# Optimization experiments

Hardware: AMD Instinct MI355X
Metric: run time of the kernel (lower is better)

## Reference

```python
import jax, jax.numpy as jnp
import numpy as np

B, C, H, W, E = 2, 4, 56, 56, 768
NH = 12
HD = E // NH
WS = 14
MLP_DIM = 3072
EPS = 1e-5


def layernorm(x, w, b):
    mu = jnp.mean(x, axis=-1, keepdims=True)
    var = jnp.mean((x - mu) ** 2, axis=-1, keepdims=True)
    return (x - mu) * jax.lax.rsqrt(var + EPS) * w + b


def setup_inputs() -> dict:
    key = jax.random.key(0)
    ks = jax.random.split(key, 12)
    s = 0.02
    return {
        "x": jax.random.normal(ks[0], (B, C, H, W, E), dtype=jnp.float32),
        "norm1_w": jnp.ones((E,), jnp.float32),
        "norm1_b": jnp.zeros((E,), jnp.float32),
        "qkv_w": jax.random.normal(ks[1], (E, 3 * E), jnp.float32) * s,
        "qkv_b": jnp.zeros((3 * E,), jnp.float32),
        "proj_w": jax.random.normal(ks[2], (E, E), jnp.float32) * s,
        "proj_b": jnp.zeros((E,), jnp.float32),
        "rel_pos_h": jax.random.normal(ks[3], (2 * WS - 1, HD), jnp.float32) * s,
        "rel_pos_w": jax.random.normal(ks[4], (2 * WS - 1, HD), jnp.float32) * s,
        "norm2_w": jnp.ones((E,), jnp.float32),
        "norm2_b": jnp.zeros((E,), jnp.float32),
        "mlp_w1": jax.random.normal(ks[5], (E, MLP_DIM), jnp.float32) * s,
        "mlp_b1": jnp.zeros((MLP_DIM,), jnp.float32),
        "mlp_w2": jax.random.normal(ks[6], (MLP_DIM, E), jnp.float32) * s,
        "mlp_b2": jnp.zeros((E,), jnp.float32),
    }


def reference(x, norm1_w, norm1_b, qkv_w, qkv_b, proj_w, proj_b,
              rel_pos_h, rel_pos_w, norm2_w, norm2_b,
              mlp_w1, mlp_b1, mlp_w2, mlp_b2):
    b, c, h, w, e = x.shape
    scale = HD ** -0.5
    shortcut = x

    y = x.reshape(b * c, h, w, e)
    y = layernorm(y, norm1_w, norm1_b)

    pad_h = (-h) % WS
    pad_w = (-w) % WS
    if pad_h or pad_w:
        y = jnp.pad(y, ((0, 0), (0, pad_h), (0, pad_w), (0, 0)))
    hp, wp = h + pad_h, w + pad_w
    y = y.reshape(b * c, hp // WS, WS, wp // WS, WS, e)
    y = y.transpose(0, 1, 3, 2, 4, 5).reshape(-1, WS, WS, e)  # [Bw, WS, WS, E]
    bw = y.shape[0]
    n = WS * WS

    # qkv projection
    qkv = y.reshape(bw, n, e) @ qkv_w + qkv_b
    qkv = qkv.reshape(bw, n, 3, NH, HD).transpose(2, 0, 3, 1, 4).reshape(3, bw * NH, n, HD)
    q, k, v = qkv[0], qkv[1], qkv[2]

    attn = (q * scale) @ jnp.swapaxes(k, -2, -1)  # [bw*NH, n, n]

    # decomposed relative position bias (q_size == k_size == WS, no interpolation)
    idx = jnp.arange(WS)[:, None] - jnp.arange(WS)[None, :] + (WS - 1)  # [WS, WS]
    Rh = rel_pos_h[idx]  # [WS, WS, HD]
    Rw = rel_pos_w[idx]
    r_q = q.reshape(-1, WS, WS, HD)
    rel_h = jnp.einsum('bhwc,hkc->bhwk', r_q, Rh)
    rel_w = jnp.einsum('bhwc,wkc->bhwk', r_q, Rw)
    attn = (attn.reshape(-1, WS, WS, WS, WS)
            + rel_h[..., :, None]
            + rel_w[:, :, :, None, :]).reshape(-1, n, n)

    attn = jax.nn.softmax(attn, axis=-1)
    out = attn @ v  # [bw*NH, n, HD]
    out = out.reshape(bw, NH, WS, WS, HD).transpose(0, 2, 3, 1, 4).reshape(bw, WS, WS, e)
    out = out @ proj_w + proj_b

    # window unpartition
    out = out.reshape(b * c, hp // WS, wp // WS, WS, WS, e)
    out = out.transpose(0, 1, 3, 2, 4, 5).reshape(b * c, hp, wp, e)
    out = out[:, :h, :w, :].reshape(b, c, h, w, e)

    x1 = shortcut + out
    z = layernorm(x1, norm2_w, norm2_b)
    z = jax.nn.gelu(z @ mlp_w1 + mlp_b1, approximate=False)
    z = z @ mlp_w2 + mlp_b2
    return x1 + z
```

## Files before the change

### kernel.cpp

```cpp
#include <hip/hip_runtime.h>
#include <math.h>

typedef unsigned short u16;
typedef __bf16 bf16x8 __attribute__((ext_vector_type(8)));
typedef float   f32x4 __attribute__((ext_vector_type(4)));
typedef u16     u16x4 __attribute__((ext_vector_type(4)));

#define TOK 25088
#define EMB 768
#define NWH 1536
#define NTOKW 196
#define PROW 224
#define PPAD 232
#define GROUP_M 4

#define OFF_VT 38535168ull
#define OFF_W0 127565824ull
#define OFF_W1 131104768ull
#define OFF_W2 132284416ull
#define OFF_W3 137003008ull
#define OFF_H  38535168ull

__device__ __forceinline__ u16 f2bf(float f) {
  __bf16 h = (__bf16)f;
  return __builtin_bit_cast(u16, h);
}

__device__ __forceinline__ float bf2f(u16 u) {
  return __builtin_bit_cast(float, (unsigned)u << 16);
}

__device__ __forceinline__ void cp16(void* lds, const void* gsrc) {
  __builtin_amdgcn_global_load_lds((const __attribute__((address_space(1))) void*)gsrc,
                                   (__attribute__((address_space(3))) void*)lds,
                                   16, 0, 0);
}

__device__ __forceinline__ f32x4 mfma16(bf16x8 a, bf16x8 b, f32x4 c) {
  return __builtin_amdgcn_mfma_f32_16x16x32_bf16(a, b, c, 0, 0, 0);
}

__device__ __forceinline__ void map_block(int b, int nwg, int nbm, int nbn,
                                          int* bm, int* bn) {
  const int q = nwg >> 3, r = nwg & 7;
  const int xcd = b & 7, slot = b >> 3;
  const int logical = (xcd < r ? xcd * (q + 1) : r * (q + 1) + (xcd - r) * q) + slot;
  const int in_group = GROUP_M * nbn;
  const int gid = logical / in_group;
  const int rem0 = logical - gid * in_group;
  const int gm = min(GROUP_M, nbm - gid * GROUP_M);
  *bm = gid * GROUP_M + rem0 % gm;
  *bn = rem0 / gm;
}

__global__ __launch_bounds__(256)
void transpose_w(const float* __restrict__ src, u16* __restrict__ dst, int R, int C) {
  __shared__ float tile[32][33];
  const int tx = threadIdx.x & 31;
  const int ty = threadIdx.x >> 5;
  const int c0 = blockIdx.x * 32;
  const int r0 = blockIdx.y * 32;
  #pragma unroll
  for (int i = ty; i < 32; i += 8)
    tile[i][tx] = src[(size_t)(r0 + i) * C + c0 + tx];
  __syncthreads();
  #pragma unroll
  for (int i = ty; i < 32; i += 8)
    dst[(size_t)(c0 + i) * R + r0 + tx] = f2bf(tile[tx][i]);
}

template<bool WIN>
__global__ __launch_bounds__(256)
void ln_kernel(const float* __restrict__ x, const float* __restrict__ g,
               const float* __restrict__ b, u16* __restrict__ y) {
  const int wave = threadIdx.x >> 6;
  const int lane = threadIdx.x & 63;
  const int row = blockIdx.x * 4 + wave;
  const float* xr = x + (size_t)row * EMB;
  float4 v[3];
  float s = 0.f, ss = 0.f;
  #pragma unroll
  for (int j = 0; j < 3; j++) {
    v[j] = *(const float4*)&xr[lane * 4 + j * 256];
    s  += v[j].x + v[j].y + v[j].z + v[j].w;
    ss += v[j].x*v[j].x + v[j].y*v[j].y + v[j].z*v[j].z + v[j].w*v[j].w;
  }
  #pragma unroll
  for (int off = 1; off < 64; off <<= 1) {
    s  += __shfl_xor(s, off);
    ss += __shfl_xor(ss, off);
  }
  const float mu = s * (1.0f / 768.0f);
  const float var = ss * (1.0f / 768.0f) - mu * mu;
  const float rs = rsqrtf(var + 1e-5f);
  size_t drow;
  if (WIN) {
    const int bc = row / 3136;
    const int rem = row - bc * 3136;
    const int h = rem / 56;
    const int w = rem - h * 56;
    const int window = bc * 16 + (h / 14) * 4 + (w / 14);
    const int token = (h % 14) * 14 + (w % 14);
    drow = (size_t)window * NTOKW + token;
  } else {
    drow = (size_t)row;
  }
  u16* yr = y + drow * EMB;
  #pragma unroll
  for (int j = 0; j < 3; j++) {
    const int e = lane * 4 + j * 256;
    const float4 gv = *(const float4*)&g[e];
    const float4 bv = *(const float4*)&b[e];
    u16x4 o;
    o[0] = f2bf((v[j].x - mu) * rs * gv.x + bv.x);
    o[1] = f2bf((v[j].y - mu) * rs * gv.y + bv.y);
    o[2] = f2bf((v[j].z - mu) * rs * gv.z + bv.z);
    o[3] = f2bf((v[j].w - mu) * rs * gv.w + bv.w);
    *(u16x4*)&yr[e] = o;
  }
}

#define EPI_QKV  0
#define EPI_PROJ 1
#define EPI_MLP1 2
#define EPI_MLP2 3

template<int EPI>
__global__ __launch_bounds__(512, 2)
void gemm256(const u16* __restrict__ A, const u16* __restrict__ Bt,
             int K, int moff, int nbm, int nbn,
             const float* __restrict__ bias,
             const float* __restrict__ aux,
             u16* __restrict__ o0, u16* __restrict__ o1, u16* __restrict__ o2,
             float* of) {
  __shared__ __align__(16) u16 lds[2][2][256 * 64];
  const int t = threadIdx.x;
  const int wave = t >> 6;
  const int lane = t & 63;
  const int quad = lane >> 4;
  const int l16 = lane & 15;
  const int wm = wave >> 2;
  const int wn = wave & 3;

  int bm, bn;
  map_block(blockIdx.x, gridDim.x, nbm, nbn, &bm, &bn);
  const int m0 = bm * 256;
  const int n0 = bn * 256;

  const int sr0 = t >> 3;
  const int sc0 = ((t ^ (t >> 3)) & 7) * 8;
  const int c1_ = t + 512;
  const int sr1 = c1_ >> 3;
  const int sc1 = ((c1_ ^ (c1_ >> 3)) & 7) * 8;
  const u16* Ag0 = A + (size_t)(m0 + sr0) * K + sc0;
  const u16* Ag1 = A + (size_t)(m0 + sr1) * K + sc1;
  const u16* Bg0 = Bt + (size_t)(n0 + sr0) * K + sc0;
  const u16* Bg1 = Bt + (size_t)(n0 + sr1) * K + sc1;
  const size_t hstep = (size_t)128 * K;

  const int cK0 = ((quad    ) ^ (l16 & 7)) * 8;
  const int cK1 = ((4 + quad) ^ (l16 & 7)) * 8;

  f32x4 acc[8][4];
  const f32x4 zero4 = {0.f, 0.f, 0.f, 0.f};
  #pragma unroll
  for (int i = 0; i < 8; i++)
    #pragma unroll
    for (int j = 0; j < 4; j++) acc[i][j] = zero4;
  bf16x8 bfr[4][2];

#define STG(bb, mat, half, G0, G1, kk) do {                                          \
    cp16(&lds[bb][mat][(half) * 8192 + wave * 512],        (G0) + (half) * hstep + (kk)); \
    cp16(&lds[bb][mat][(half) * 8192 + 4096 + wave * 512], (G1) + (half) * hstep + (kk)); \
  } while (0)

#define LOADB(bb) do {                                                               \
    _Pragma("unroll")                                                                \
    for (int nf = 0; nf < 4; nf++) {                                                 \
      bfr[nf][0] = *(const bf16x8*)&lds[bb][1][(wn * 64 + nf * 16 + l16) * 64 + cK0];\
      bfr[nf][1] = *(const bf16x8*)&lds[bb][1][(wn * 64 + nf * 16 + l16) * 64 + cK1];\
    }                                                                                \
  } while (0)

#define PHASE(bb, slab, PRE, POST) do {                                              \
    const int ar_ = (wm * 128 + (slab) * 32 + l16) * 64;                             \
    bf16x8 a00 = *(const bf16x8*)&lds[bb][0][ar_ + cK0];                             \
    bf16x8 a01 = *(const bf16x8*)&lds[bb][0][ar_ + cK1];                             \
    bf16x8 a10 = *(const bf16x8*)&lds[bb][0][ar_ + 1024 + cK0];                      \
    bf16x8 a11 = *(const bf16x8*)&lds[bb][0][ar_ + 1024 + cK1];                      \
    PRE;                                                                             \
    __builtin_amdgcn_s_barrier();                                                    \
    asm volatile("s_waitcnt lgkmcnt(0)" ::: "memory");                               \
    __builtin_amdgcn_sched_barrier(0);                                               \
    __builtin_amdgcn_s_setprio(1);                                                   \
    _Pragma("unroll")                                                                \
    for (int nf = 0; nf < 4; nf++) {                                                 \
      acc[(slab) * 2    ][nf] = mfma16(a00, bfr[nf][0], acc[(slab) * 2    ][nf]);    \
      acc[(slab) * 2    ][nf] = mfma16(a01, bfr[nf][1], acc[(slab) * 2    ][nf]);    \
      acc[(slab) * 2 + 1][nf] = mfma16(a10, bfr[nf][0], acc[(slab) * 2 + 1][nf]);    \
      acc[(slab) * 2 + 1][nf] = mfma16(a11, bfr[nf][1], acc[(slab) * 2 + 1][nf]);    \
    }                                                                                \
    __builtin_amdgcn_s_setprio(0);                                                   \
    POST;                                                                            \
    __builtin_amdgcn_s_barrier();                                                    \
  } while (0)

  STG(0, 1, 0, Bg0, Bg1, 0);  STG(0, 1, 1, Bg0, Bg1, 0);
  STG(0, 0, 0, Ag0, Ag1, 0);  STG(0, 0, 1, Ag0, Ag1, 0);
  STG(1, 1, 0, Bg0, Bg1, 64); STG(1, 1, 1, Bg0, Bg1, 64);
  asm volatile("s_waitcnt vmcnt(4)" ::: "memory");
  __builtin_amdgcn_s_barrier();

  const int T = K >> 7;
  for (int it = 0; it < T; ++it) {
    const bool nlast = (it < T - 1);
    const int kA1 = (2 * it + 1) << 6;
    const int kT2 = (2 * it + 2) << 6;
    const int kT3 = (2 * it + 3) << 6;

    LOADB(0);
    PHASE(0, 0, STG(1, 0, 0, Ag0, Ag1, kA1), );
    PHASE(0, 1, STG(1, 0, 1, Ag0, Ag1, kA1), );
    PHASE(0, 2, if (nlast) STG(0, 1, 0, Bg0, Bg1, kT2), );
    PHASE(0, 3, if (nlast) STG(0, 1, 1, Bg0, Bg1, kT2),
          if (nlast) { asm volatile("s_waitcnt vmcnt(4)" ::: "memory"); }
          else       { asm volatile("s_waitcnt vmcnt(0)" ::: "memory"); }
          __builtin_amdgcn_sched_barrier(0); );
    LOADB(1);
    PHASE(1, 0, if (nlast) STG(0, 0, 0, Ag0, Ag1, kT2), );
    PHASE(1, 1, if (nlast) STG(0, 0, 1, Ag0, Ag1, kT2), );
    PHASE(1, 2, if (nlast) STG(1, 1, 0, Bg0, Bg1, kT3), );
    PHASE(1, 3, if (nlast) STG(1, 1, 1, Bg0, Bg1, kT3),
          asm volatile("s_waitcnt vmcnt(4)" ::: "memory");
          __builtin_amdgcn_sched_barrier(0); );
  }
#undef STG
#undef LOADB
#undef PHASE

  #pragma unroll
  for (int mf = 0; mf < 8; mf++) {
    const int mb = m0 + wm * 128 + mf * 16 + quad * 4;
    #pragma unroll
    for (int nf = 0; nf < 4; nf++) {
      const int n = n0 + wn * 64 + nf * 16 + l16;
      const float bn_ = bias[n];
      if (EPI == EPI_QKV) {
        const int j3 = n / 768;
        const int rem = n - j3 * 768;
        const int head = rem >> 6;
        const int d = rem & 63;
        if (j3 == 2) {
          const int window = mb / 196;
          const int token = mb - window * 196;
          const int wh = window * 12 + head;
          u16x4 pv;
          #pragma unroll
          for (int r = 0; r < 4; r++) pv[r] = f2bf(acc[mf][nf][r] + bn_);
          *(u16x4*)&o2[((size_t)wh * 64 + d) * PROW + token] = pv;
        } else {
          u16* dst = (j3 == 0) ? o0 : o1;
          #pragma unroll
          for (int r = 0; r < 4; r++) {
            const int m = mb + r;
            const int window = m / 196;
            const int token = m - window * 196;
            const int wh = window * 12 + head;
            dst[((size_t)wh * NTOKW + token) * 64 + d] = f2bf(acc[mf][nf][r] + bn_);
          }
        }
      } else if (EPI == EPI_MLP1) {
        #pragma unroll
        for (int r = 0; r < 4; r++) {
          const int m = mb + r;
          float v = acc[mf][nf][r] + bn_;
          v = 0.5f * v * (1.0f + erff(v * 0.70710678118654752f));
          o0[(size_t)m * 3072 + n] = f2bf(v);
        }
      }
    }
  }
}

template<int EPI>
__global__ __launch_bounds__(256, 3)
void gemm_bt(const u16* __restrict__ A, const u16* __restrict__ Bt,
             int K, int moff, int nbm, int nbn,
             const float* __restrict__ bias,
             const float* __restrict__ aux,
             u16* __restrict__ o0,
             float* of) {
  __shared__ __align__(16) u16 lsA[4096];
  __shared__ __align__(16) u16 lsB[4096];
  const int t = threadIdx.x;
  const int wave = t >> 6;
  const int lane = t & 63;
  const int quad = lane >> 4;
  const int l16 = lane & 15;

  int bm, bn;
  map_block(blockIdx.x, gridDim.x, nbm, nbn, &bm, &bn);
  const int m0 = bm * 128;
  const int n0 = bn * 128;

  const int wm = (wave >> 1) * 64;
  const int wn = (wave & 1) * 64;

  const int srow = t >> 2;
  const int scol = (((t & 3) ^ ((t >> 3) & 3))) * 8;
  const u16* Ag = A + (size_t)(m0 + srow) * K + scol;
  const u16* Bg = Bt + (size_t)(n0 + srow) * K + scol;
  u16* lA0 = lsA + wave * 512;
  u16* lA1 = lsA + 2048 + wave * 512;
  u16* lB0 = lsB + wave * 512;
  u16* lB1 = lsB + 2048 + wave * 512;

  const int kc = (quad ^ ((l16 >> 1) & 3)) * 8;

  f32x4 acc[4][4];
  const f32x4 zero4 = {0.f, 0.f, 0.f, 0.f};
  #pragma unroll
  for (int i = 0; i < 4; i++)
    #pragma unroll
    for (int j = 0; j < 4; j++) acc[i][j] = zero4;

  for (int k0 = 0; k0 < K; k0 += 32) {
    cp16(lA0, Ag + k0);
    cp16(lA1, Ag + (size_t)64 * K + k0);
    cp16(lB0, Bg + k0);
    cp16(lB1, Bg + (size_t)64 * K + k0);
    __syncthreads();
    bf16x8 af[4], bfr[4];
    #pragma unroll
    for (int i = 0; i < 4; i++)
      af[i] = *(const bf16x8*)&lsA[(wm + i * 16 + l16) * 32 + kc];
    #pragma unroll
    for (int j = 0; j < 4; j++)
      bfr[j] = *(const bf16x8*)&lsB[(wn + j * 16 + l16) * 32 + kc];
    #pragma unroll
    for (int i = 0; i < 4; i++)
      #pragma unroll
      for (int j = 0; j < 4; j++)
        acc[i][j] = mfma16(af[i], bfr[j], acc[i][j]);
    __syncthreads();
  }

  #pragma unroll
  for (int i = 0; i < 4; i++) {
    const int mb = m0 + wm + i * 16 + quad * 4;
    #pragma unroll
    for (int j = 0; j < 4; j++) {
      const int n = n0 + wn + j * 16 + l16;
      const float bn_ = bias[n];
      if (EPI == EPI_PROJ) {
        #pragma unroll
        for (int r = 0; r < 4; r++) {
          const int m = mb + r;
          const int window = m / 196;
          const int token = m - window * 196;
          const int bc = window >> 4;
          const int wi = window & 15;
          const int th = token / 14;
          const int tw = token - th * 14;
          const int h = (wi >> 2) * 14 + th;
          const int w = (wi & 3) * 14 + tw;
          const size_t flat = (((size_t)bc * 56 + h) * 56 + w) * 768 + n;
          of[flat] = acc[i][j][r] + bn_ + aux[flat];
        }
      } else {
        #pragma unroll
        for (int r = 0; r < 4; r++) {
          const int m = mb + r + moff;
          const size_t idx = (size_t)m * 768 + n;
          of[idx] = acc[i][j][r] + bn_ + aux[idx];
        }
      }
    }
  }
}

__global__ __launch_bounds__(256, 2)
void attn_fused(const u16* __restrict__ q, const u16* __restrict__ k,
                const u16* __restrict__ vT,
                const float* __restrict__ rph, const float* __restrict__ rpw,
                u16* __restrict__ out) {
  __shared__ __align__(16) u16 lsK[208 * 64];
  __shared__ __align__(16) u16 relh[16 * 224];
  __shared__ __align__(16) u16 relw[16 * 224];
  __shared__ __align__(16) u16 lsP[4][16 * PPAD];
  const int t = threadIdx.x;
  const int wave = t >> 6;
  const int lane = t & 63;
  const int quad = lane >> 4;
  const int l16 = lane & 15;
  const int wh = blockIdx.x;
  const u16* qg = q + (size_t)wh * (NTOKW * 64);
  const u16* kg = k + (size_t)wh * (NTOKW * 64);
  const u16* vg = vT + (size_t)wh * 64 * PROW;
  const int window = wh / 12;
  const int head = wh - window * 12;

  #pragma unroll
  for (int i = 0; i < 6; i++) {
    const int chunk = i * 256 + t;
    const int goff = ((chunk & ~7) | ((chunk ^ (chunk >> 3)) & 7)) * 8;
    cp16(lsK + (i * 256 + wave * 64) * 8, kg + goff);
  }
  if (t < 32) {
    const int chunk = 1536 + t;
    const int goff = ((chunk & ~7) | ((chunk ^ (chunk >> 3)) & 7)) * 8;
    cp16(lsK + 1536 * 8, kg + goff);
  }

  const f32x4 zero4 = {0.f, 0.f, 0.f, 0.f};
  for (int tile = wave; tile < 14; tile += 4) {
    f32x4 ah = zero4, aw = zero4;
    const int ridx = min(max(tile - l16 + 13, 0), 26);
    #pragma unroll
    for (int ks = 0; ks < 2; ks++) {
      const int ko = ks * 32 + quad * 8;
      bf16x8 aq_h = *(const bf16x8*)&qg[(tile * 14 + l16) * 64 + ko];
      bf16x8 aq_w = *(const bf16x8*)&qg[(tile + 14 * l16) * 64 + ko];
      bf16x8 bh, bw;
      const float* ph = rph + ridx * 64 + ko;
      const float* pw = rpw + ridx * 64 + ko;
      #pragma unroll
      for (int e = 0; e < 8; e++) { bh[e] = (__bf16)ph[e]; bw[e] = (__bf16)pw[e]; }
      ah = mfma16(aq_h, bh, ah);
      aw = mfma16(aq_w, bw, aw);
    }
    #pragma unroll
    for (int r = 0; r < 4; r++) {
      const int m = quad * 4 + r;
      if (m < 14) {
        relh[l16 * 224 + tile * 14 + m] = f2bf(ah[r]);
        relw[l16 * 224 + tile + 14 * m] = f2bf(aw[r]);
      }
    }
  }
  __syncthreads();

  const float scale = 0.125f;
  const int sw = l16 & 7;
  u16* myP = &lsP[wave][0];
  for (int s = wave; s < 13; s += 4) {
    bf16x8 aq[2];
    #pragma unroll
    for (int ks = 0; ks < 2; ks++)
      aq[ks] = *(const bf16x8*)&qg[(s * 16 + l16) * 64 + ks * 32 + quad * 8];
    f32x4 acc[13];
    #pragma unroll
    for (int jt = 0; jt < 13; jt++) {
      f32x4 a = zero4;
      a = mfma16(aq[0], *(const bf16x8*)&lsK[(jt * 16 + l16) * 64 + (quad ^ sw) * 8], a);
      a = mfma16(aq[1], *(const bf16x8*)&lsK[(jt * 16 + l16) * 64 + ((quad + 4) ^ sw) * 8], a);
      acc[jt] = a;
    }
    f32x4 mx = {-1e30f, -1e30f, -1e30f, -1e30f};
    #pragma unroll
    for (int jt = 0; jt < 13; jt++) {
      const int col = jt * 16 + l16;
      if (col < 196) {
        const int kh = col / 14;
        const int kw = col - kh * 14;
        const u16x4 rhu = *(const u16x4*)&relh[kh * 224 + s * 16 + quad * 4];
        const u16x4 rwu = *(const u16x4*)&relw[kw * 224 + s * 16 + quad * 4];
        #pragma unroll
        for (int r = 0; r < 4; r++)
          acc[jt][r] = acc[jt][r] * scale + bf2f(rhu[r]) + bf2f(rwu[r]);
      } else {
        acc[jt] = (f32x4){-1e30f, -1e30f, -1e30f, -1e30f};
      }
      #pragma unroll
      for (int r = 0; r < 4; r++) mx[r] = fmaxf(mx[r], acc[jt][r]);
    }
    #pragma unroll
    for (int off = 1; off < 16; off <<= 1)
      #pragma unroll
      for (int r = 0; r < 4; r++) mx[r] = fmaxf(mx[r], __shfl_xor(mx[r], off));
    f32x4 sum = zero4;
    #pragma unroll
    for (int jt = 0; jt < 13; jt++)
      #pragma unroll
      for (int r = 0; r < 4; r++) {
        const float p = exp2f((acc[jt][r] - mx[r]) * 1.4426950408889634f);
        acc[jt][r] = p;
        sum[r] += p;
      }
    #pragma unroll
    for (int off = 1; off < 16; off <<= 1)
      #pragma unroll
      for (int r = 0; r < 4; r++) sum[r] += __shfl_xor(sum[r], off);
    #pragma unroll
    for (int r = 0; r < 4; r++) {
      const float rinv = 1.0f / sum[r];
      const int prow = (quad * 4 + r) * PPAD;
      #pragma unroll
      for (int jt = 0; jt < 13; jt++)
        myP[prow + jt * 16 + l16] = f2bf(acc[jt][r] * rinv);
      myP[prow + 208 + l16] = 0;
    }
    asm volatile("s_waitcnt lgkmcnt(0)" ::: "memory");
    f32x4 acco[4] = {zero4, zero4, zero4, zero4};
    #pragma unroll
    for (int ks = 0; ks < 7; ks++) {
      bf16x8 ap = *(const bf16x8*)&myP[l16 * PPAD + ks * 32 + quad * 8];
      #pragma unroll
      for (int nt = 0; nt < 4; nt++) {
        bf16x8 bv = *(const bf16x8*)&vg[(nt * 16 + l16) * PROW + ks * 32 + quad * 8];
        acco[nt] = mfma16(ap, bv, acco[nt]);
      }
    }
    #pragma unroll
    for (int nt = 0; nt < 4; nt++)
      #pragma unroll
      for (int r = 0; r < 4; r++) {
        const int i = s * 16 + quad * 4 + r;
        if (i < 196)
          out[((size_t)window * NTOKW + i) * EMB + head * 64 + nt * 16 + l16] =
              f2bf(acco[nt][r]);
      }
  }
}

extern "C" void kernel_launch(void* const* d_in, const int* in_sizes, int n_in,
                              void* d_out, int out_size, void* d_ws, size_t ws_size,
                              hipStream_t stream) {
  const float* x      = (const float*)d_in[0];
  const float* n1w    = (const float*)d_in[1];
  const float* n1b    = (const float*)d_in[2];
  const float* qkv_w  = (const float*)d_in[3];
  const float* qkv_b  = (const float*)d_in[4];
  const float* proj_w = (const float*)d_in[5];
  const float* proj_b = (const float*)d_in[6];
  const float* rph    = (const float*)d_in[7];
  const float* rpw    = (const float*)d_in[8];
  const float* n2w    = (const float*)d_in[9];
  const float* n2b    = (const float*)d_in[10];
  const float* w1     = (const float*)d_in[11];
  const float* b1     = (const float*)d_in[12];
  const float* w2     = (const float*)d_in[13];
  const float* b2     = (const float*)d_in[14];
  float* out = (float*)d_out;

  char* ws = (char*)d_ws;
  u16* bufT   = (u16*)(ws);
  u16* vTb    = (u16*)(ws + OFF_VT);
  u16* hb     = (u16*)(ws + OFF_H);
  u16* wqkvT  = (u16*)(ws + OFF_W0);
  u16* wprojT = (u16*)(ws + OFF_W1);
  u16* w1T    = (u16*)(ws + OFF_W2);
  u16* w2T    = (u16*)(ws + OFF_W3);
  u16* qb = (u16*)d_out;
  u16* kb = qb + (size_t)19267584;

  dim3 blk(256), blkg(512);
  transpose_w<<<dim3(72, 24), blk, 0, stream>>>(qkv_w, wqkvT, 768, 2304);
  transpose_w<<<dim3(24, 24), blk, 0, stream>>>(proj_w, wprojT, 768, 768);
  transpose_w<<<dim3(96, 24), blk, 0, stream>>>(w1, w1T, 768, 3072);
  transpose_w<<<dim3(24, 96), blk, 0, stream>>>(w2, w2T, 3072, 768);

  ln_kernel<true><<<6272, blk, 0, stream>>>(x, n1w, n1b, bufT);

  gemm256<EPI_QKV><<<98 * 9, blkg, 0, stream>>>(
      bufT, wqkvT, 768, 0, 98, 9, qkv_b, nullptr, qb, kb, vTb, nullptr);

  attn_fused<<<NWH, blk, 0, stream>>>(qb, kb, vTb, rph, rpw, bufT);

  gemm_bt<EPI_PROJ><<<196 * 6, blk, 0, stream>>>(
      bufT, wprojT, 768, 0, 196, 6, proj_b, x, nullptr, out);

  ln_kernel<false><<<6272, blk, 0, stream>>>(out, n2w, n2b, bufT);

  for (int c = 0; c < 2; c++) {
    const int row0 = c * 12544;
    gemm256<EPI_MLP1><<<49 * 12, blkg, 0, stream>>>(
        bufT + (size_t)row0 * 768, w1T, 768, 0, 49, 12, b1, nullptr, hb, nullptr, nullptr, nullptr);
    gemm_bt<EPI_MLP2><<<98 * 6, blk, 0, stream>>>(
        hb, w2T, 3072, row0, 98, 6, b2, out, nullptr, out);
  }

  (void)in_sizes; (void)n_in; (void)out_size; (void)ws_size;
}
```

Before: 955.5 us.

## Replace pipelined 256x256 GEMM with simple 128x128 BK=64 kernel for all GEMMs

Removes the heavily pipelined 256x256-tile, 512-thread double-buffered GEMM used for QKV and MLP1. All four GEMMs now use one single-buffered 128x128 tile kernel, and that kernel's K step grows from 32 to 64. The intent is to simplify the code, raise occupancy, and halve barrier count per K for proj and MLP2. The cost is the loss of software pipelining that overlapped global loads with MFMA, and lower data reuse per tile for the large GEMMs.

```diff
diff --git a/kernel.cpp b/kernel.cpp
--- a/kernel.cpp
+++ b/kernel.cpp
@@ -126,124 +126,78 @@
 #define EPI_MLP2 3
 
 template<int EPI>
-__global__ __launch_bounds__(512, 2)
-void gemm256(const u16* __restrict__ A, const u16* __restrict__ Bt,
-             int K, int moff, int nbm, int nbn,
-             const float* __restrict__ bias,
-             const float* __restrict__ aux,
-             u16* __restrict__ o0, u16* __restrict__ o1, u16* __restrict__ o2,
-             float* of) {
-  __shared__ __align__(16) u16 lds[2][2][256 * 64];
+__global__ __launch_bounds__(256, 3)
+void gemm_bt64(const u16* __restrict__ A, const u16* __restrict__ Bt,
+               int K, int moff, int nbm, int nbn,
+               const float* __restrict__ bias,
+               const float* __restrict__ aux,
+               u16* __restrict__ o0, u16* __restrict__ o1, u16* __restrict__ o2,
+               float* of) {
+  __shared__ __align__(16) u16 lsA[8192];
+  __shared__ __align__(16) u16 lsB[8192];
   const int t = threadIdx.x;
   const int wave = t >> 6;
   const int lane = t & 63;
   const int quad = lane >> 4;
   const int l16 = lane & 15;
-  const int wm = wave >> 2;
-  const int wn = wave & 3;
 
   int bm, bn;
   map_block(blockIdx.x, gridDim.x, nbm, nbn, &bm, &bn);
-  const int m0 = bm * 256;
-  const int n0 = bn * 256;
-
-  const int sr0 = t >> 3;
-  const int sc0 = ((t ^ (t >> 3)) & 7) * 8;
-  const int c1_ = t + 512;
-  const int sr1 = c1_ >> 3;
-  const int sc1 = ((c1_ ^ (c1_ >> 3)) & 7) * 8;
-  const u16* Ag0 = A + (size_t)(m0 + sr0) * K + sc0;
-  const u16* Ag1 = A + (size_t)(m0 + sr1) * K + sc1;
-  const u16* Bg0 = Bt + (size_t)(n0 + sr0) * K + sc0;
-  const u16* Bg1 = Bt + (size_t)(n0 + sr1) * K + sc1;
-  const size_t hstep = (size_t)128 * K;
+  const int m0 = bm * 128;
+  const int n0 = bn * 128;
+
+  const int wm = (wave >> 1) * 64;
+  const int wn = (wave & 1) * 64;
+
+  const int sr = t >> 3;
+  const int sc = ((t ^ (t >> 3)) & 7) * 8;
+  const u16* Ag = A + (size_t)(m0 + sr) * K + sc;
+  const u16* Bg = Bt + (size_t)(n0 + sr) * K + sc;
+  u16* dA = lsA + wave * 512;
+  u16* dB = lsB + wave * 512;
 
   const int cK0 = ((quad    ) ^ (l16 & 7)) * 8;
   const int cK1 = ((4 + quad) ^ (l16 & 7)) * 8;
 
-  f32x4 acc[8][4];
+  f32x4 acc[4][4];
   const f32x4 zero4 = {0.f, 0.f, 0.f, 0.f};
   #pragma unroll
-  for (int i = 0; i < 8; i++)
+  for (int i = 0; i < 4; i++)
     #pragma unroll
     for (int j = 0; j < 4; j++) acc[i][j] = zero4;
-  bf16x8 bfr[4][2];
-
-#define STG(bb, mat, half, G0, G1, kk) do {                                          \
-    cp16(&lds[bb][mat][(half) * 8192 + wave * 512],        (G0) + (half) * hstep + (kk)); \
-    cp16(&lds[bb][mat][(half) * 8192 + 4096 + wave * 512], (G1) + (half) * hstep + (kk)); \
-  } while (0)
-
-#define LOADB(bb) do {                                                               \
-    _Pragma("unroll")                                                                \
-    for (int nf = 0; nf < 4; nf++) {                                                 \
-      bfr[nf][0] = *(const bf16x8*)&lds[bb][1][(wn * 64 + nf * 16 + l16) * 64 + cK0];\
-      bfr[nf][1] = *(const bf16x8*)&lds[bb][1][(wn * 64 + nf * 16 + l16) * 64 + cK1];\
-    }                                                                                \
-  } while (0)
-
-#define PHASE(bb, slab, PRE, POST) do {                                              \
-    const int ar_ = (wm * 128 + (slab) * 32 + l16) * 64;                             \
-    bf16x8 a00 = *(const bf16x8*)&lds[bb][0][ar_ + cK0];                             \
-    bf16x8 a01 = *(const bf16x8*)&lds[bb][0][ar_ + cK1];                             \
-    bf16x8 a10 = *(const bf16x8*)&lds[bb][0][ar_ + 1024 + cK0];                      \
-    bf16x8 a11 = *(const bf16x8*)&lds[bb][0][ar_ + 1024 + cK1];                      \
-    PRE;                                                                             \
-    __builtin_amdgcn_s_barrier();                                                    \
-    asm volatile("s_waitcnt lgkmcnt(0)" ::: "memory");                               \
-    __builtin_amdgcn_sched_barrier(0);                                               \
-    __builtin_amdgcn_s_setprio(1);                                                   \
-    _Pragma("unroll")                                                                \
-    for (int nf = 0; nf < 4; nf++) {                                                 \
-      acc[(slab) * 2    ][nf] = mfma16(a00, bfr[nf][0], acc[(slab) * 2    ][nf]);    \
-      acc[(slab) * 2    ][nf] = mfma16(a01, bfr[nf][1], acc[(slab) * 2    ][nf]);    \
-      acc[(slab) * 2 + 1][nf] = mfma16(a10, bfr[nf][0], acc[(slab) * 2 + 1][nf]);    \
-      acc[(slab) * 2 + 1][nf] = mfma16(a11, bfr[nf][1], acc[(slab) * 2 + 1][nf]);    \
-    }                                                                                \
-    __builtin_amdgcn_s_setprio(0);                                                   \
-    POST;                                                                            \
-    __builtin_amdgcn_s_barrier();                                                    \
-  } while (0)
-
-  STG(0, 1, 0, Bg0, Bg1, 0);  STG(0, 1, 1, Bg0, Bg1, 0);
-  STG(0, 0, 0, Ag0, Ag1, 0);  STG(0, 0, 1, Ag0, Ag1, 0);
-  STG(1, 1, 0, Bg0, Bg1, 64); STG(1, 1, 1, Bg0, Bg1, 64);
-  asm volatile("s_waitcnt vmcnt(4)" ::: "memory");
-  __builtin_amdgcn_s_barrier();
-
-  const int T = K >> 7;
-  for (int it = 0; it < T; ++it) {
-    const bool nlast = (it < T - 1);
-    const int kA1 = (2 * it + 1) << 6;
-    const int kT2 = (2 * it + 2) << 6;
-    const int kT3 = (2 * it + 3) << 6;
-
-    LOADB(0);
-    PHASE(0, 0, STG(1, 0, 0, Ag0, Ag1, kA1), );
-    PHASE(0, 1, STG(1, 0, 1, Ag0, Ag1, kA1), );
-    PHASE(0, 2, if (nlast) STG(0, 1, 0, Bg0, Bg1, kT2), );
-    PHASE(0, 3, if (nlast) STG(0, 1, 1, Bg0, Bg1, kT2),
-          if (nlast) { asm volatile("s_waitcnt vmcnt(4)" ::: "memory"); }
-          else       { asm volatile("s_waitcnt vmcnt(0)" ::: "memory"); }
-          __builtin_amdgcn_sched_barrier(0); );
-    LOADB(1);
-    PHASE(1, 0, if (nlast) STG(0, 0, 0, Ag0, Ag1, kT2), );
-    PHASE(1, 1, if (nlast) STG(0, 0, 1, Ag0, Ag1, kT2), );
-    PHASE(1, 2, if (nlast) STG(1, 1, 0, Bg0, Bg1, kT3), );
-    PHASE(1, 3, if (nlast) STG(1, 1, 1, Bg0, Bg1, kT3),
-          asm volatile("s_waitcnt vmcnt(4)" ::: "memory");
-          __builtin_amdgcn_sched_barrier(0); );
-  }
-#undef STG
-#undef LOADB
-#undef PHASE
-
-  #pragma unroll
-  for (int mf = 0; mf < 8; mf++) {
-    const int mb = m0 + wm * 128 + mf * 16 + quad * 4;
-    #pragma unroll
-    for (int nf = 0; nf < 4; nf++) {
-      const int n = n0 + wn * 64 + nf * 16 + l16;
+
+  for (int k0 = 0; k0 < K; k0 += 64) {
+    #pragma unroll
+    for (int i = 0; i < 4; i++) {
+      cp16(dA + i * 2048, Ag + (size_t)(32 * i) * K + k0);
+      cp16(dB + i * 2048, Bg + (size_t)(32 * i) * K + k0);
+    }
+    __syncthreads();
+    #pragma unroll
+    for (int ks = 0; ks < 2; ks++) {
+      const int kc = ks ? cK1 : cK0;
+      bf16x8 af[4], bfr[4];
+      #pragma unroll
+      for (int i = 0; i < 4; i++)
+        af[i] = *(const bf16x8*)&lsA[(wm + i * 16 + l16) * 64 + kc];
+      #pragma unroll
+      for (int j = 0; j < 4; j++)
+        bfr[j] = *(const bf16x8*)&lsB[(wn + j * 16 + l16) * 64 + kc];
+      #pragma unroll
+      for (int i = 0; i < 4; i++)
+        #pragma unroll
+        for (int j = 0; j < 4; j++)
+          acc[i][j] = mfma16(af[i], bfr[j], acc[i][j]);
+    }
+    __syncthreads();
+  }
+
+  #pragma unroll
+  for (int i = 0; i < 4; i++) {
+    const int mb = m0 + wm + i * 16 + quad * 4;
+    #pragma unroll
+    for (int j = 0; j < 4; j++) {
+      const int n = n0 + wn + j * 16 + l16;
       const float bn_ = bias[n];
       if (EPI == EPI_QKV) {
         const int j3 = n / 768;
@@ -256,7 +210,7 @@
           const int wh = window * 12 + head;
           u16x4 pv;
           #pragma unroll
-          for (int r = 0; r < 4; r++) pv[r] = f2bf(acc[mf][nf][r] + bn_);
+          for (int r = 0; r < 4; r++) pv[r] = f2bf(acc[i][j][r] + bn_);
           *(u16x4*)&o2[((size_t)wh * 64 + d) * PROW + token] = pv;
         } else {
           u16* dst = (j3 == 0) ? o0 : o1;
@@ -266,93 +220,10 @@
             const int window = m / 196;
             const int token = m - window * 196;
             const int wh = window * 12 + head;
-            dst[((size_t)wh * NTOKW + token) * 64 + d] = f2bf(acc[mf][nf][r] + bn_);
+            dst[((size_t)wh * NTOKW + token) * 64 + d] = f2bf(acc[i][j][r] + bn_);
           }
         }
-      } else if (EPI == EPI_MLP1) {
-        #pragma unroll
-        for (int r = 0; r < 4; r++) {
-          const int m = mb + r;
-          float v = acc[mf][nf][r] + bn_;
-          v = 0.5f * v * (1.0f + erff(v * 0.70710678118654752f));
-          o0[(size_t)m * 3072 + n] = f2bf(v);
-        }
-      }
-    }
-  }
-}
-
-template<int EPI>
-__global__ __launch_bounds__(256, 3)
-void gemm_bt(const u16* __restrict__ A, const u16* __restrict__ Bt,
-             int K, int moff, int nbm, int nbn,
-             const float* __restrict__ bias,
-             const float* __restrict__ aux,
-             u16* __restrict__ o0,
-             float* of) {
-  __shared__ __align__(16) u16 lsA[4096];
-  __shared__ __align__(16) u16 lsB[4096];
-  const int t = threadIdx.x;
-  const int wave = t >> 6;
-  const int lane = t & 63;
-  const int quad = lane >> 4;
-  const int l16 = lane & 15;
-
-  int bm, bn;
-  map_block(blockIdx.x, gridDim.x, nbm, nbn, &bm, &bn);
-  const int m0 = bm * 128;
-  const int n0 = bn * 128;
-
-  const int wm = (wave >> 1) * 64;
-  const int wn = (wave & 1) * 64;
-
-  const int srow = t >> 2;
-  const int scol = (((t & 3) ^ ((t >> 3) & 3))) * 8;
-  const u16* Ag = A + (size_t)(m0 + srow) * K + scol;
-  const u16* Bg = Bt + (size_t)(n0 + srow) * K + scol;
-  u16* lA0 = lsA + wave * 512;
-  u16* lA1 = lsA + 2048 + wave * 512;
-  u16* lB0 = lsB + wave * 512;
-  u16* lB1 = lsB + 2048 + wave * 512;
-
-  const int kc = (quad ^ ((l16 >> 1) & 3)) * 8;
-
-  f32x4 acc[4][4];
-  const f32x4 zero4 = {0.f, 0.f, 0.f, 0.f};
-  #pragma unroll
-  for (int i = 0; i < 4; i++)
-    #pragma unroll
-    for (int j = 0; j < 4; j++) acc[i][j] = zero4;
-
-  for (int k0 = 0; k0 < K; k0 += 32) {
-    cp16(lA0, Ag + k0);
-    cp16(lA1, Ag + (size_t)64 * K + k0);
-    cp16(lB0, Bg + k0);
-    cp16(lB1, Bg + (size_t)64 * K + k0);
-    __syncthreads();
-    bf16x8 af[4], bfr[4];
-    #pragma unroll
-    for (int i = 0; i < 4; i++)
-      af[i] = *(const bf16x8*)&lsA[(wm + i * 16 + l16) * 32 + kc];
-    #pragma unroll
-    for (int j = 0; j < 4; j++)
-      bfr[j] = *(const bf16x8*)&lsB[(wn + j * 16 + l16) * 32 + kc];
-    #pragma unroll
-    for (int i = 0; i < 4; i++)
-      #pragma unroll
-      for (int j = 0; j < 4; j++)
-        acc[i][j] = mfma16(af[i], bfr[j], acc[i][j]);
-    __syncthreads();
-  }
-
-  #pragma unroll
-  for (int i = 0; i < 4; i++) {
-    const int mb = m0 + wm + i * 16 + quad * 4;
-    #pragma unroll
-    for (int j = 0; j < 4; j++) {
-      const int n = n0 + wn + j * 16 + l16;
-      const float bn_ = bias[n];
-      if (EPI == EPI_PROJ) {
+      } else if (EPI == EPI_PROJ) {
         #pragma unroll
         for (int r = 0; r < 4; r++) {
           const int m = mb + r;
@@ -366,6 +237,14 @@
           const int w = (wi & 3) * 14 + tw;
           const size_t flat = (((size_t)bc * 56 + h) * 56 + w) * 768 + n;
           of[flat] = acc[i][j][r] + bn_ + aux[flat];
+        }
+      } else if (EPI == EPI_MLP1) {
+        #pragma unroll
+        for (int r = 0; r < 4; r++) {
+          const int m = mb + r;
+          float v = acc[i][j][r] + bn_;
+          v = 0.5f * v * (1.0f + erff(v * 0.70710678118654752f));
+          o0[(size_t)m * 3072 + n] = f2bf(v);
         }
       } else {
         #pragma unroll
@@ -554,7 +433,7 @@
   u16* qb = (u16*)d_out;
   u16* kb = qb + (size_t)19267584;
 
-  dim3 blk(256), blkg(512);
+  dim3 blk(256);
   transpose_w<<<dim3(72, 24), blk, 0, stream>>>(qkv_w, wqkvT, 768, 2304);
   transpose_w<<<dim3(24, 24), blk, 0, stream>>>(proj_w, wprojT, 768, 768);
   transpose_w<<<dim3(96, 24), blk, 0, stream>>>(w1, w1T, 768, 3072);
@@ -562,22 +441,22 @@
 
   ln_kernel<true><<<6272, blk, 0, stream>>>(x, n1w, n1b, bufT);
 
-  gemm256<EPI_QKV><<<98 * 9, blkg, 0, stream>>>(
-      bufT, wqkvT, 768, 0, 98, 9, qkv_b, nullptr, qb, kb, vTb, nullptr);
+  gemm_bt64<EPI_QKV><<<196 * 18, blk, 0, stream>>>(
+      bufT, wqkvT, 768, 0, 196, 18, qkv_b, nullptr, qb, kb, vTb, nullptr);
 
   attn_fused<<<NWH, blk, 0, stream>>>(qb, kb, vTb, rph, rpw, bufT);
 
-  gemm_bt<EPI_PROJ><<<196 * 6, blk, 0, stream>>>(
-      bufT, wprojT, 768, 0, 196, 6, proj_b, x, nullptr, out);
+  gemm_bt64<EPI_PROJ><<<196 * 6, blk, 0, stream>>>(
+      bufT, wprojT, 768, 0, 196, 6, proj_b, x, nullptr, nullptr, nullptr, out);
 
   ln_kernel<false><<<6272, blk, 0, stream>>>(out, n2w, n2b, bufT);
 
   for (int c = 0; c < 2; c++) {
     const int row0 = c * 12544;
-    gemm256<EPI_MLP1><<<49 * 12, blkg, 0, stream>>>(
-        bufT + (size_t)row0 * 768, w1T, 768, 0, 49, 12, b1, nullptr, hb, nullptr, nullptr, nullptr);
-    gemm_bt<EPI_MLP2><<<98 * 6, blk, 0, stream>>>(
-        hb, w2T, 3072, row0, 98, 6, b2, out, nullptr, out);
+    gemm_bt64<EPI_MLP1><<<98 * 24, blk, 0, stream>>>(
+        bufT + (size_t)row0 * 768, w1T, 768, 0, 98, 24, b1, nullptr, hb, nullptr, nullptr, nullptr);
+    gemm_bt64<EPI_MLP2><<<98 * 6, blk, 0, stream>>>(
+        hb, w2T, 3072, row0, 98, 6, b2, out, nullptr, nullptr, nullptr, out);
   }
 
   (void)in_sizes; (void)n_in; (void)out_size; (void)ws_size;
```

After: 844.7 us. 1.13x faster.
